# Performance work log

Measured on AMD Instinct MI355X. Metric: run time of the kernel, lower is better.

## Reference

```python
import jax, jax.numpy as jnp
import numpy as np

EMBD = 256
HEAD = 4
HD = EMBD // HEAD  # 64
EPS = 1e-5


def setup_inputs() -> dict:
    key = jax.random.key(0)
    ks = jax.random.split(key, 12)
    s = lambda fan_in: 1.0 / np.sqrt(fan_in)
    return {
        "x": jax.random.normal(ks[0], (16, 1024, EMBD), dtype=jnp.float32),
        # attention params (stored as [in, out])
        "qkv_w": jax.random.uniform(ks[1], (EMBD, 3 * EMBD), jnp.float32, -s(EMBD), s(EMBD)),
        "qkv_b": jax.random.uniform(ks[2], (3 * EMBD,), jnp.float32, -s(EMBD), s(EMBD)),
        "out_w": jax.random.uniform(ks[3], (EMBD, EMBD), jnp.float32, -s(EMBD), s(EMBD)),
        "out_b": jax.random.uniform(ks[4], (EMBD,), jnp.float32, -s(EMBD), s(EMBD)),
        # MLP params
        "fc_w": jax.random.uniform(ks[5], (EMBD, 4 * EMBD), jnp.float32, -s(EMBD), s(EMBD)),
        "fc_b": jax.random.uniform(ks[6], (4 * EMBD,), jnp.float32, -s(EMBD), s(EMBD)),
        "proj_w": jax.random.uniform(ks[7], (4 * EMBD, EMBD), jnp.float32, -s(4 * EMBD), s(4 * EMBD)),
        "proj_b": jax.random.uniform(ks[8], (EMBD,), jnp.float32, -s(4 * EMBD), s(4 * EMBD)),
        # LayerNorm params
        "ln1_g": jnp.ones((EMBD,), jnp.float32),
        "ln1_b": jnp.zeros((EMBD,), jnp.float32),
        "ln2_g": jnp.ones((EMBD,), jnp.float32),
        "ln2_b": jnp.zeros((EMBD,), jnp.float32),
    }


def layer_norm(x, g, b):
    mu = jnp.mean(x, axis=-1, keepdims=True)
    var = jnp.mean(jnp.square(x - mu), axis=-1, keepdims=True)
    return (x - mu) * jax.lax.rsqrt(var + EPS) * g + b


def block_forward(x, qkv_w, qkv_b, out_w, out_b, fc_w, fc_b, proj_w, proj_b,
                  ln1_g, ln1_b, ln2_g, ln2_b):
    B, S, E = x.shape
    # --- attention branch ---
    h = layer_norm(x, ln1_g, ln1_b)
    qkv = h @ qkv_w + qkv_b                       # [B,S,3E]
    q, k, v = jnp.split(qkv, 3, axis=-1)
    q = q.reshape(B, S, HEAD, HD).transpose(0, 2, 1, 3)  # [B,H,S,D]
    k = k.reshape(B, S, HEAD, HD).transpose(0, 2, 1, 3)
    v = v.reshape(B, S, HEAD, HD).transpose(0, 2, 1, 3)
    att = jnp.einsum('bhqd,bhkd->bhqk', q, k) / jnp.sqrt(jnp.float32(HD))
    causal = jnp.tril(jnp.ones((S, S), dtype=bool))
    att = jnp.where(causal, att, -jnp.inf)
    att = jax.nn.softmax(att, axis=-1)
    o = jnp.einsum('bhqk,bhkd->bhqd', att, v)     # [B,H,S,D]
    o = o.transpose(0, 2, 1, 3).reshape(B, S, E)
    x = x + o @ out_w + out_b
    # --- MLP branch (dropout inactive at eval) ---
    h = layer_norm(x, ln2_g, ln2_b)
    h = jax.nn.relu(h @ fc_w + fc_b)
    x = x + h @ proj_w + proj_b
    return x


def reference(x, qkv_w, qkv_b, out_w, out_b, fc_w, fc_b, proj_w, proj_b,
              ln1_g, ln1_b, ln2_g, ln2_b):
    return block_forward(x, qkv_w, qkv_b, out_w, out_b, fc_w, fc_b,
                         proj_w, proj_b, ln1_g, ln1_b, ln2_g, ln2_b)
```

## Files before the change

kernel.cpp:

```cpp
#include <hip/hip_runtime.h>
#include <cstdint>


using f32x4 = __attribute__((ext_vector_type(4))) float;
using s16x8 = __attribute__((ext_vector_type(8))) short;
using s16x4 = __attribute__((ext_vector_type(4))) short;

__device__ inline short f2bf(float f) {
    union { float f; unsigned u; } v{f};
    unsigned r = (v.u + 0x7FFFu + ((v.u >> 16) & 1u)) >> 16;
    return (short)r;
}

__device__ inline int cvt_pk_bf16(float lo, float hi) {
    int d;
    asm("v_cvt_pk_bf16_f32 %0, %1, %2" : "=v"(d) : "v"(lo), "v"(hi));
    return d;
}
__device__ inline void swap32(int& a, int& b) {
    asm("v_permlane32_swap_b32 %0, %1" : "+v"(a), "+v"(b));
}
__device__ inline void swap16(int& a, int& b) {
    asm("v_permlane16_swap_b32 %0, %1" : "+v"(a), "+v"(b));
}

__device__ inline void gload16(const void* g, void* l) {
    __builtin_amdgcn_global_load_lds(
        (const __attribute__((address_space(1))) void*)g,
        (__attribute__((address_space(3))) void*)l, 16, 0, 0);
}

__global__ __launch_bounds__(256) void wconv_all_kernel(
    const float* __restrict__ qkv_w, const float* __restrict__ out_w,
    const float* __restrict__ fc_w,  const float* __restrict__ proj_w,
    short* __restrict__ wt_qkv, short* __restrict__ wt_out,
    short* __restrict__ wt_fc,  short* __restrict__ wt_proj)
{
    __shared__ short T[64][65];
    int id = blockIdx.x;
    const float* W; short* Wt; int K, N, nt, kt;
    if (id < 48)       { W = qkv_w;  Wt = wt_qkv;  K = 256;  N = 768;  nt = id % 12;        kt = id / 12; }
    else if (id < 64)  { W = out_w;  Wt = wt_out;  K = 256;  N = 256;  nt = (id - 48) & 3;  kt = (id - 48) >> 2; }
    else if (id < 128) { W = fc_w;   Wt = wt_fc;   K = 256;  N = 1024; nt = (id - 64) & 15; kt = (id - 64) >> 4; }
    else               { W = proj_w; Wt = wt_proj; K = 1024; N = 256;  nt = (id - 128) & 3; kt = (id - 128) >> 2; }
    int n0 = nt * 64, k0 = kt * 64;

    int tid = threadIdx.x;
    int r  = tid >> 2;
    int c  = (tid & 3) << 4;

    const float* src = W + (size_t)(k0 + r) * N + n0 + c;
#pragma unroll
    for (int u = 0; u < 4; ++u) {
        float4 v = *reinterpret_cast<const float4*>(src + u * 4);
        T[r][c + u * 4 + 0] = f2bf(v.x);
        T[r][c + u * 4 + 1] = f2bf(v.y);
        T[r][c + u * 4 + 2] = f2bf(v.z);
        T[r][c + u * 4 + 3] = f2bf(v.w);
    }
    __syncthreads();
    s16x8 o0, o1;
#pragma unroll
    for (int j = 0; j < 8; ++j) { o0[j] = T[c + j][r]; o1[j] = T[c + 8 + j][r]; }
    short* dst = Wt + (size_t)(n0 + r) * K + k0 + c;
    *reinterpret_cast<s16x8*>(dst)     = o0;
    *reinterpret_cast<s16x8*>(dst + 8) = o1;
}

__global__ __launch_bounds__(256) void ln_kernel(const float* __restrict__ x,
                                                 const float* __restrict__ gamma,
                                                 const float* __restrict__ beta,
                                                 short* __restrict__ out)
{
    int tid  = threadIdx.x;
    int lane = tid & 63;
    int row  = blockIdx.x * 4 + (tid >> 6);
    const float* xr = x + (size_t)row * 256;
    float4 v = *reinterpret_cast<const float4*>(xr + lane * 4);

    float s = v.x + v.y + v.z + v.w;
#pragma unroll
    for (int o = 32; o >= 1; o >>= 1) s += __shfl_xor(s, o);
    float mu = s * (1.0f / 256.0f);

    float dx = v.x - mu, dy = v.y - mu, dz = v.z - mu, dw = v.w - mu;
    float q = dx * dx + dy * dy + dz * dz + dw * dw;
#pragma unroll
    for (int o = 32; o >= 1; o >>= 1) q += __shfl_xor(q, o);
    float rstd = rsqrtf(q * (1.0f / 256.0f) + 1e-5f);

    float4 gv = *reinterpret_cast<const float4*>(gamma + lane * 4);
    float4 bv = *reinterpret_cast<const float4*>(beta + lane * 4);
    s16x4 ov;
    ov[0] = f2bf(dx * rstd * gv.x + bv.x);
    ov[1] = f2bf(dy * rstd * gv.y + bv.y);
    ov[2] = f2bf(dz * rstd * gv.z + bv.z);
    ov[3] = f2bf(dw * rstd * gv.w + bv.w);
    *reinterpret_cast<s16x4*>(out + (size_t)row * 256 + lane * 4) = ov;
}

template <int RELU, int RES, int OBF16, int BM>
__global__ __launch_bounds__(256) void mgemm_kernel(const short* __restrict__ A,
                                                    const short* __restrict__ Bt,
                                                    const float* __restrict__ bias,
                                                    const float* __restrict__ R,
                                                    void* __restrict__ Cv,
                                                    int N, int K)
{
    constexpr int MI = BM / 32;
    __shared__ short As[BM * 64];
    __shared__ short Bs[128 * 64];

    int tid = threadIdx.x;
    int l   = tid & 63;
    int w   = tid >> 6;
    int lr  = l & 15;
    int lk8 = (l >> 4) << 3;
    int r4  = (l >> 4) << 2;
    int wr  = w >> 1, wc = w & 1;
    int bn  = blockIdx.x * 128, bm = blockIdx.y * BM;

    int scolS = ((l & 7) << 3) ^ ((l >> 3) << 3);
    int srowA = w * (BM / 4) + (l >> 3);
    int srowB = (w << 5) + (l >> 3);
    const short* pa = A  + (size_t)(bm + srowA) * K + scolS;
    const short* pb = Bt + (size_t)(bn + srowB) * K + scolS;
    short* dstA = As + w * (BM / 4) * 64;
    short* dstB = Bs + (w << 11);

    f32x4 acc[MI][4];
#pragma unroll
    for (int mi = 0; mi < MI; ++mi)
#pragma unroll
        for (int ni = 0; ni < 4; ++ni) acc[mi][ni] = (f32x4){0.f, 0.f, 0.f, 0.f};

    int swz = (lr & 7) << 3;

    for (int k0 = 0; k0 < K; k0 += 64) {
        __syncthreads();
#pragma unroll
        for (int i = 0; i < BM / 32; ++i)
            gload16(pa + (size_t)(i * 8) * K + k0, dstA + (i << 9));
#pragma unroll
        for (int i = 0; i < 4; ++i)
            gload16(pb + (size_t)(i * 8) * K + k0, dstB + (i << 9));
        __syncthreads();

#pragma unroll
        for (int ks = 0; ks < 2; ++ks) {
            s16x8 af[MI], bf[4];
#pragma unroll
            for (int mi = 0; mi < MI; ++mi) {
                int row = wr * (BM / 2) + (mi << 4) + lr;
                af[mi] = *reinterpret_cast<const s16x8*>(
                    &As[(row << 6) + (((ks << 5) + lk8) ^ swz)]);
            }
#pragma unroll
            for (int ni = 0; ni < 4; ++ni) {
                int row = (wc << 6) + (ni << 4) + lr;
                bf[ni] = *reinterpret_cast<const s16x8*>(
                    &Bs[(row << 6) + (((ks << 5) + lk8) ^ swz)]);
            }
#pragma unroll
            for (int mi = 0; mi < MI; ++mi)
#pragma unroll
                for (int ni = 0; ni < 4; ++ni)
                    acc[mi][ni] = __builtin_amdgcn_mfma_f32_16x16x32_bf16(
                        af[mi], bf[ni], acc[mi][ni], 0, 0, 0);
        }
    }

    float bv[4];
#pragma unroll
    for (int ni = 0; ni < 4; ++ni)
        bv[ni] = bias[bn + (wc << 6) + (ni << 4) + lr];

#pragma unroll
    for (int mi = 0; mi < MI; ++mi) {
#pragma unroll
        for (int ni = 0; ni < 4; ++ni) {
            int n = bn + (wc << 6) + (ni << 4) + lr;
#pragma unroll
            for (int r = 0; r < 4; ++r) {
                int m = bm + wr * (BM / 2) + (mi << 4) + r4 + r;
                float v = acc[mi][ni][r] + bv[ni];
                if (RELU) v = fmaxf(v, 0.0f);
                if (RES)  v += R[(size_t)m * N + n];
                if (OBF16) ((short*)Cv)[(size_t)m * N + n] = f2bf(v);
                else       ((float*)Cv)[(size_t)m * N + n] = v;
            }
        }
    }
}

__global__ __launch_bounds__(256) void oproj_ln_kernel(const short* __restrict__ A,
                                                       const short* __restrict__ Bt,
                                                       const float* __restrict__ bias,
                                                       const float* __restrict__ R,
                                                       float* __restrict__ x1,
                                                       short* __restrict__ h2,
                                                       const float* __restrict__ g,
                                                       const float* __restrict__ bb)
{
    __shared__ short As[64 * 64];
    __shared__ short Bs[256 * 64];

    int tid = threadIdx.x;
    int l   = tid & 63;
    int w   = tid >> 6;
    int lr  = l & 15;
    int lk8 = (l >> 4) << 3;
    int r4  = (l >> 4) << 2;
    int bm  = blockIdx.x * 64;

    int scolS = ((l & 7) << 3) ^ ((l >> 3) << 3);
    const short* pa = A  + (size_t)(bm + (w << 4) + (l >> 3)) * 256 + scolS;
    const short* pb = Bt + (size_t)((w << 6) + (l >> 3)) * 256 + scolS;
    short* dstA = As + (w << 10);
    short* dstB = Bs + (w << 12);

    f32x4 acc[16];
#pragma unroll
    for (int ni = 0; ni < 16; ++ni) acc[ni] = (f32x4){0.f, 0.f, 0.f, 0.f};

    int swz = (lr & 7) << 3;

    for (int k0 = 0; k0 < 256; k0 += 64) {
        __syncthreads();
#pragma unroll
        for (int i = 0; i < 2; ++i)
            gload16(pa + (size_t)(i * 8) * 256 + k0, dstA + (i << 9));
#pragma unroll
        for (int i = 0; i < 8; ++i)
            gload16(pb + (size_t)(i * 8) * 256 + k0, dstB + (i << 9));
        __syncthreads();

#pragma unroll
        for (int ks = 0; ks < 2; ++ks) {
            int arow = (w << 4) + lr;
            s16x8 af = *reinterpret_cast<const s16x8*>(
                &As[(arow << 6) + (((ks << 5) + lk8) ^ swz)]);
#pragma unroll
            for (int ni = 0; ni < 16; ++ni) {
                int row = (ni << 4) + lr;
                s16x8 bf = *reinterpret_cast<const s16x8*>(
                    &Bs[(row << 6) + (((ks << 5) + lk8) ^ swz)]);
                acc[ni] = __builtin_amdgcn_mfma_f32_16x16x32_bf16(af, bf, acc[ni], 0, 0, 0);
            }
        }
    }

#pragma unroll
    for (int ni = 0; ni < 16; ++ni) {
        int n = (ni << 4) + lr;
        float bvx = bias[n];
#pragma unroll
        for (int r = 0; r < 4; ++r) {
            int m = bm + (w << 4) + r4 + r;
            acc[ni][r] += bvx + R[(size_t)m * 256 + n];
        }
    }
#pragma unroll
    for (int r = 0; r < 4; ++r) {
        float s = 0.0f;
#pragma unroll
        for (int ni = 0; ni < 16; ++ni) s += acc[ni][r];
        s += __shfl_xor(s, 1); s += __shfl_xor(s, 2);
        s += __shfl_xor(s, 4); s += __shfl_xor(s, 8);
        float mu = s * (1.0f / 256.0f);
        float q = 0.0f;
#pragma unroll
        for (int ni = 0; ni < 16; ++ni) {
            float d = acc[ni][r] - mu;
            q += d * d;
        }
        q += __shfl_xor(q, 1); q += __shfl_xor(q, 2);
        q += __shfl_xor(q, 4); q += __shfl_xor(q, 8);
        float rstd = rsqrtf(q * (1.0f / 256.0f) + 1e-5f);

        int m = bm + (w << 4) + r4 + r;
#pragma unroll
        for (int ni = 0; ni < 16; ++ni) {
            int n = (ni << 4) + lr;
            float v = acc[ni][r];
            x1[(size_t)m * 256 + n] = v;
            h2[(size_t)m * 256 + n] = f2bf((v - mu) * rstd * g[n] + bb[n]);
        }
    }
}

__global__ __launch_bounds__(256, 4) void attn_kernel(const short* __restrict__ qkv,
                                                      short* __restrict__ o)
{
    __shared__ short Qs[64 * 64];
    __shared__ short Ks[128 * 64];
    __shared__ short Vt[2 * 64 * 64];

    int bid  = blockIdx.x;
    int xcd  = bid & 7;
    int rest = bid >> 3;
    int qt   = rest & 15;
    int bh   = ((rest >> 4) << 3) | xcd;
    int b = bh >> 2, h = bh & 3;

    int tid = threadIdx.x;
    const short* base = qkv + (size_t)b * 1024 * 768;

    int l   = tid & 63;
    int w   = tid >> 6;
    int lr  = l & 15;
    int g   = l >> 4;
    int lk8 = g << 3;
    int w16 = w << 4;
    int qglob = qt * 64 + w16 + lr;

    const float SC = 0.125f * 1.44269504088896f;

    {
        int qr = tid >> 2;
        int c0 = (tid & 3) << 4;
        int sw = (qr & 7) << 3;
        const short* qg = base + (size_t)(qt * 64 + qr) * 768 + h * 64 + c0;
        s16x8 q0 = *reinterpret_cast<const s16x8*>(qg);
        s16x8 q1 = *reinterpret_cast<const s16x8*>(qg + 8);
        *reinterpret_cast<s16x8*>(&Qs[qr * 64 + (c0 ^ sw)])       = q0;
        *reinterpret_cast<s16x8*>(&Qs[qr * 64 + ((c0 + 8) ^ sw)]) = q1;
    }
    __syncthreads();

    s16x8 qf[2];
#pragma unroll
    for (int ks = 0; ks < 2; ++ks) {
        int row = w16 + lr;
        qf[ks] = *reinterpret_cast<const s16x8*>(
            &Qs[row * 64 + ((32 * ks + lk8) ^ ((lr & 7) << 3))]);
    }

    float m = -1e30f, lsum = 0.0f;
    f32x4 oacc[4];
#pragma unroll
    for (int dt = 0; dt < 4; ++dt) oacc[dt] = (f32x4){0.f, 0.f, 0.f, 0.f};

    int ntile = qt >> 1;
    for (int kt = 0; kt <= ntile; ++kt) {
        __syncthreads();
        {
            int c0 = (tid & 3) << 4;
#pragma unroll
            for (int i = 0; i < 2; ++i) {
                int krow = i * 64 + (tid >> 2);
                const short* kg = base + (size_t)(kt * 128 + krow) * 768 + 256 + h * 64 + c0;
                s16x8 k0v = *reinterpret_cast<const s16x8*>(kg);
                s16x8 k1v = *reinterpret_cast<const s16x8*>(kg + 8);
                int sw = (krow & 7) << 3;
                *reinterpret_cast<s16x8*>(&Ks[krow * 64 + (c0 ^ sw)])       = k0v;
                *reinterpret_cast<s16x8*>(&Ks[krow * 64 + ((c0 + 8) ^ sw)]) = k1v;
                s16x8 v0 = *reinterpret_cast<const s16x8*>(kg + 256);
                s16x8 v1 = *reinterpret_cast<const s16x8*>(kg + 264);
                short* vth = Vt + ((krow >> 6) << 12);
                int kkl = krow & 63;
#pragma unroll
                for (int e = 0; e < 8; ++e) {
                    int da = c0 + e, db = c0 + 8 + e;
                    vth[da * 64 + (kkl ^ ((da & 7) << 3))] = v0[e];
                    vth[db * 64 + (kkl ^ ((db & 7) << 3))] = v1[e];
                }
            }
        }
        __syncthreads();

        f32x4 s[8];
#pragma unroll
        for (int jt = 0; jt < 8; ++jt) s[jt] = (f32x4){0.f, 0.f, 0.f, 0.f};
#pragma unroll
        for (int ks = 0; ks < 2; ++ks) {
#pragma unroll
            for (int jt = 0; jt < 8; ++jt) {
                int row = jt * 16 + lr;
                s16x8 kf = *reinterpret_cast<const s16x8*>(
                    &Ks[row * 64 + ((32 * ks + lk8) ^ ((lr & 7) << 3))]);
                s[jt] = __builtin_amdgcn_mfma_f32_16x16x32_bf16(kf, qf[ks], s[jt], 0, 0, 0);
            }
        }
#pragma unroll
        for (int jt = 0; jt < 8; ++jt)
#pragma unroll
            for (int r = 0; r < 4; ++r) s[jt][r] *= SC;

        if (kt == ntile) {
#pragma unroll
            for (int jt = 0; jt < 8; ++jt) {
                int kb = kt * 128 + jt * 16 + 4 * g;
#pragma unroll
                for (int r = 0; r < 4; ++r)
                    if (kb + r > qglob) s[jt][r] = -1e30f;
            }
        }

        float rm = fmaxf(fmaxf(s[0][0], s[0][1]), fmaxf(s[0][2], s[0][3]));
#pragma unroll
        for (int jt = 1; jt < 8; ++jt) {
            float t = fmaxf(fmaxf(s[jt][0], s[jt][1]), fmaxf(s[jt][2], s[jt][3]));
            rm = fmaxf(rm, t);
        }
        rm = fmaxf(rm, __shfl_xor(rm, 16));
        rm = fmaxf(rm, __shfl_xor(rm, 32));
        float mn  = fmaxf(m, rm);
        float fct = exp2f(m - mn);
        m = mn;
        float ps = 0.0f;
#pragma unroll
        for (int jt = 0; jt < 8; ++jt) {
#pragma unroll
            for (int r = 0; r < 4; ++r) {
                float p = exp2f(s[jt][r] - mn);
                s[jt][r] = p;
                ps += p;
            }
        }
        ps += __shfl_xor(ps, 16);
        ps += __shfl_xor(ps, 32);
        lsum = lsum * fct + ps;

        int cpk[8][2];
#pragma unroll
        for (int jt = 0; jt < 8; ++jt) {
            cpk[jt][0] = cvt_pk_bf16(s[jt][0], s[jt][1]);
            cpk[jt][1] = cvt_pk_bf16(s[jt][2], s[jt][3]);
        }

#pragma unroll
        for (int r = 0; r < 4; ++r) {
            float f4 = __shfl(fct, 4 * g + r);
#pragma unroll
            for (int dt = 0; dt < 4; ++dt) oacc[dt][r] *= f4;
        }

#pragma unroll
        for (int ks = 0; ks < 4; ++ks) {
            int a0 = cpk[2 * ks][0],     a1 = cpk[2 * ks][1];
            int b0 = cpk[2 * ks + 1][0], b1 = cpk[2 * ks + 1][1];
            swap32(a0, b0); swap32(a1, b1);
            swap16(a0, b0); swap16(a1, b1);
            union { int i[4]; s16x8 v; } fr;
            fr.i[0] = a0; fr.i[1] = a1; fr.i[2] = b0; fr.i[3] = b1;
            const short* vth = Vt + ((ks >> 1) << 12);
#pragma unroll
            for (int dt = 0; dt < 4; ++dt) {
                int vrow = dt * 16 + lr;
                s16x8 vf = *reinterpret_cast<const s16x8*>(
                    &vth[vrow * 64 + ((((ks & 1) << 5) + lk8) ^ ((lr & 7) << 3))]);
                oacc[dt] = __builtin_amdgcn_mfma_f32_16x16x32_bf16(fr.v, vf, oacc[dt], 0, 0, 0);
            }
        }
    }

#pragma unroll
    for (int r = 0; r < 4; ++r) {
        float lv  = __shfl(lsum, 4 * g + r);
        float inv = 1.0f / lv;
        short* orow = o + (size_t)(b * 1024 + qt * 64 + w16 + 4 * g + r) * 256 + h * 64;
#pragma unroll
        for (int dt = 0; dt < 4; ++dt)
            orow[dt * 16 + lr] = f2bf(oacc[dt][r] * inv);
    }
}

extern "C" void kernel_launch(void* const* d_in, const int* in_sizes, int n_in,
                              void* d_out, int out_size, void* d_ws, size_t ws_size,
                              hipStream_t stream)
{
    const float* x      = (const float*)d_in[0];
    const float* qkv_w  = (const float*)d_in[1];
    const float* qkv_b  = (const float*)d_in[2];
    const float* out_w  = (const float*)d_in[3];
    const float* out_b  = (const float*)d_in[4];
    const float* fc_w   = (const float*)d_in[5];
    const float* fc_b   = (const float*)d_in[6];
    const float* proj_w = (const float*)d_in[7];
    const float* proj_b = (const float*)d_in[8];
    const float* ln1_g  = (const float*)d_in[9];
    const float* ln1_b  = (const float*)d_in[10];
    const float* ln2_g  = (const float*)d_in[11];
    const float* ln2_b  = (const float*)d_in[12];
    float* out = (float*)d_out;

    short* ws = (short*)d_ws;
    short* wt_qkv  = ws;
    short* wt_out  = ws + 196608;
    short* wt_fc   = ws + 262144;
    short* wt_proj = ws + 524288;
    short* bufA    = ws + 786432;
    short* bufB    = ws + 4980736;

    dim3 blk(256);

    wconv_all_kernel<<<dim3(192), blk, 0, stream>>>(
        qkv_w, out_w, fc_w, proj_w, wt_qkv, wt_out, wt_fc, wt_proj);
    ln_kernel<<<dim3(4096), blk, 0, stream>>>(x, ln1_g, ln1_b, bufA);
    mgemm_kernel<0, 0, 1, 128><<<dim3(6, 128), blk, 0, stream>>>(
        bufA, wt_qkv, qkv_b, nullptr, bufB, 768, 256);
    attn_kernel<<<dim3(1024), blk, 0, stream>>>(bufB, bufA);
    oproj_ln_kernel<<<dim3(256), blk, 0, stream>>>(
        bufA, wt_out, out_b, x, out, bufA, ln2_g, ln2_b);
    mgemm_kernel<1, 0, 1, 128><<<dim3(8, 128), blk, 0, stream>>>(
        bufA, wt_fc, fc_b, nullptr, bufB, 1024, 256);
    mgemm_kernel<0, 1, 0, 64><<<dim3(2, 256), blk, 0, stream>>>(
        bufB, wt_proj, proj_b, out, out, 256, 1024);
}
```

Baseline: 137.6 us.

## Restructure causal attention with pre-transposed V, paired q-tiles, and double-buffered K/V

The QKV GEMM epilogue now writes Q/K into a 512-wide buffer and V directly transposed per head. This removes the scalar in-kernel V transpose into LDS. The attention kernel processes a balanced pair of query tiles (qt and 15-qt) per block and reads Q fragments straight from global memory. It uses 64-key tiles double-buffered in LDS via async global-to-LDS loads (gload16) so the next tile's load overlaps compute. The costs are fewer blocks, lower occupancy (launch bounds 2), and strided scattered bf16 stores for V in the GEMM epilogue.

```diff
diff --git a/kernel.cpp b/kernel.cpp
--- a/kernel.cpp
+++ b/kernel.cpp
@@ -99,12 +99,13 @@
     *reinterpret_cast<s16x4*>(out + (size_t)row * 256 + lane * 4) = ov;
 }
 
-template <int RELU, int RES, int OBF16, int BM>
+template <int RELU, int RES, int OBF16, int BM, int QKV>
 __global__ __launch_bounds__(256) void mgemm_kernel(const short* __restrict__ A,
                                                     const short* __restrict__ Bt,
                                                     const float* __restrict__ bias,
                                                     const float* __restrict__ R,
                                                     void* __restrict__ Cv,
+                                                    short* __restrict__ vt,
                                                     int N, int K)
 {
     constexpr int MI = BM / 32;
@@ -186,8 +187,19 @@
                 float v = acc[mi][ni][r] + bv[ni];
                 if (RELU) v = fmaxf(v, 0.0f);
                 if (RES)  v += R[(size_t)m * N + n];
-                if (OBF16) ((short*)Cv)[(size_t)m * N + n] = f2bf(v);
-                else       ((float*)Cv)[(size_t)m * N + n] = v;
+                if (QKV) {
+                    if (bn < 512) {
+                        ((short*)Cv)[(size_t)m * 512 + n] = f2bf(v);
+                    } else {
+                        int hh = (n - 512) >> 6, dd = (n - 512) & 63;
+                        int bb = m >> 10, ss = m & 1023;
+                        vt[(size_t)((((bb << 2) | hh) << 6) | dd) * 1024 + ss] = f2bf(v);
+                    }
+                } else if (OBF16) {
+                    ((short*)Cv)[(size_t)m * N + n] = f2bf(v);
+                } else {
+                    ((float*)Cv)[(size_t)m * N + n] = v;
+                }
             }
         }
     }
@@ -289,180 +301,169 @@
     }
 }
 
-__global__ __launch_bounds__(256, 4) void attn_kernel(const short* __restrict__ qkv,
+__global__ __launch_bounds__(256, 2) void attn_kernel(const short* __restrict__ qk,
+                                                      const short* __restrict__ vt,
                                                       short* __restrict__ o)
 {
-    __shared__ short Qs[64 * 64];
-    __shared__ short Ks[128 * 64];
-    __shared__ short Vt[2 * 64 * 64];
+    __shared__ short Ks[2][64 * 64];
+    __shared__ short Vs[2][64 * 64];
 
     int bid  = blockIdx.x;
     int xcd  = bid & 7;
-    int rest = bid >> 3;
-    int qt   = rest & 15;
-    int bh   = ((rest >> 4) << 3) | xcd;
+    int pair = (bid >> 3) & 7;
+    int bhg  = bid >> 6;
+    int bh   = (bhg << 3) | xcd;
     int b = bh >> 2, h = bh & 3;
 
     int tid = threadIdx.x;
-    const short* base = qkv + (size_t)b * 1024 * 768;
-
     int l   = tid & 63;
     int w   = tid >> 6;
     int lr  = l & 15;
     int g   = l >> 4;
     int lk8 = g << 3;
     int w16 = w << 4;
-    int qglob = qt * 64 + w16 + lr;
+
+    int srow = (w << 3) + (l >> 3);
+    int scol = ((l & 7) << 3) ^ (((l >> 3) & 7) << 3);
+    const short* kgp = qk + (size_t)(b * 1024 + srow) * 512 + 256 + h * 64 + scol;
+    const short* vgp = vt + (size_t)((bh << 6) + srow) * 1024 + scol;
+    short* dstK = &Ks[0][(w << 3) * 64];
+    short* dstV = &Vs[0][(w << 3) * 64];
+    const int BUFS = 64 * 64;
 
     const float SC = 0.125f * 1.44269504088896f;
-
-    {
-        int qr = tid >> 2;
-        int c0 = (tid & 3) << 4;
-        int sw = (qr & 7) << 3;
-        const short* qg = base + (size_t)(qt * 64 + qr) * 768 + h * 64 + c0;
-        s16x8 q0 = *reinterpret_cast<const s16x8*>(qg);
-        s16x8 q1 = *reinterpret_cast<const s16x8*>(qg + 8);
-        *reinterpret_cast<s16x8*>(&Qs[qr * 64 + (c0 ^ sw)])       = q0;
-        *reinterpret_cast<s16x8*>(&Qs[qr * 64 + ((c0 + 8) ^ sw)]) = q1;
-    }
-    __syncthreads();
-
-    s16x8 qf[2];
-#pragma unroll
-    for (int ks = 0; ks < 2; ++ks) {
-        int row = w16 + lr;
-        qf[ks] = *reinterpret_cast<const s16x8*>(
-            &Qs[row * 64 + ((32 * ks + lk8) ^ ((lr & 7) << 3))]);
-    }
-
-    float m = -1e30f, lsum = 0.0f;
-    f32x4 oacc[4];
-#pragma unroll
-    for (int dt = 0; dt < 4; ++dt) oacc[dt] = (f32x4){0.f, 0.f, 0.f, 0.f};
-
-    int ntile = qt >> 1;
-    for (int kt = 0; kt <= ntile; ++kt) {
+    int rsw = (lr & 7) << 3;
+
+    int cur = 1;
+    for (int sel = 0; sel < 2; ++sel) {
+        int qt = sel == 0 ? pair : 15 - pair;
+
+        const short* qrow = qk + (size_t)(b * 1024 + qt * 64 + w16 + lr) * 512 + h * 64;
+        s16x8 qf[2];
+        qf[0] = *reinterpret_cast<const s16x8*>(qrow + lk8);
+        qf[1] = *reinterpret_cast<const s16x8*>(qrow + 32 + lk8);
+
+#pragma unroll
+        for (int i = 0; i < 2; ++i) {
+            gload16(kgp + (size_t)(qt * 0 + i * 32) * 512, dstK + (cur ^ 1) * BUFS + (i << 11));
+            gload16(vgp + (size_t)(i * 32) * 1024,         dstV + (cur ^ 1) * BUFS + (i << 11));
+        }
         __syncthreads();
-        {
-            int c0 = (tid & 3) << 4;
-#pragma unroll
-            for (int i = 0; i < 2; ++i) {
-                int krow = i * 64 + (tid >> 2);
-                const short* kg = base + (size_t)(kt * 128 + krow) * 768 + 256 + h * 64 + c0;
-                s16x8 k0v = *reinterpret_cast<const s16x8*>(kg);
-                s16x8 k1v = *reinterpret_cast<const s16x8*>(kg + 8);
-                int sw = (krow & 7) << 3;
-                *reinterpret_cast<s16x8*>(&Ks[krow * 64 + (c0 ^ sw)])       = k0v;
-                *reinterpret_cast<s16x8*>(&Ks[krow * 64 + ((c0 + 8) ^ sw)]) = k1v;
-                s16x8 v0 = *reinterpret_cast<const s16x8*>(kg + 256);
-                s16x8 v1 = *reinterpret_cast<const s16x8*>(kg + 264);
-                short* vth = Vt + ((krow >> 6) << 12);
-                int kkl = krow & 63;
-#pragma unroll
-                for (int e = 0; e < 8; ++e) {
-                    int da = c0 + e, db = c0 + 8 + e;
-                    vth[da * 64 + (kkl ^ ((da & 7) << 3))] = v0[e];
-                    vth[db * 64 + (kkl ^ ((db & 7) << 3))] = v1[e];
+        cur ^= 1;
+
+        float m = -1e30f, lsum = 0.0f;
+        f32x4 oacc[4];
+#pragma unroll
+        for (int dt = 0; dt < 4; ++dt) oacc[dt] = (f32x4){0.f, 0.f, 0.f, 0.f};
+        int qglob = qt * 64 + w16 + lr;
+
+        for (int kt = 0; kt <= qt; ++kt) {
+            if (kt < qt) {
+#pragma unroll
+                for (int i = 0; i < 2; ++i) {
+                    gload16(kgp + (size_t)((kt + 1) * 64 + i * 32) * 512,
+                            dstK + (cur ^ 1) * BUFS + (i << 11));
+                    gload16(vgp + (size_t)(i * 32) * 1024 + (kt + 1) * 64,
+                            dstV + (cur ^ 1) * BUFS + (i << 11));
                 }
             }
-        }
-        __syncthreads();
-
-        f32x4 s[8];
-#pragma unroll
-        for (int jt = 0; jt < 8; ++jt) s[jt] = (f32x4){0.f, 0.f, 0.f, 0.f};
-#pragma unroll
-        for (int ks = 0; ks < 2; ++ks) {
-#pragma unroll
-            for (int jt = 0; jt < 8; ++jt) {
-                int row = jt * 16 + lr;
-                s16x8 kf = *reinterpret_cast<const s16x8*>(
-                    &Ks[row * 64 + ((32 * ks + lk8) ^ ((lr & 7) << 3))]);
-                s[jt] = __builtin_amdgcn_mfma_f32_16x16x32_bf16(kf, qf[ks], s[jt], 0, 0, 0);
-            }
-        }
-#pragma unroll
-        for (int jt = 0; jt < 8; ++jt)
-#pragma unroll
-            for (int r = 0; r < 4; ++r) s[jt][r] *= SC;
-
-        if (kt == ntile) {
-#pragma unroll
-            for (int jt = 0; jt < 8; ++jt) {
-                int kb = kt * 128 + jt * 16 + 4 * g;
-#pragma unroll
-                for (int r = 0; r < 4; ++r)
-                    if (kb + r > qglob) s[jt][r] = -1e30f;
-            }
-        }
-
-        float rm = fmaxf(fmaxf(s[0][0], s[0][1]), fmaxf(s[0][2], s[0][3]));
-#pragma unroll
-        for (int jt = 1; jt < 8; ++jt) {
-            float t = fmaxf(fmaxf(s[jt][0], s[jt][1]), fmaxf(s[jt][2], s[jt][3]));
-            rm = fmaxf(rm, t);
-        }
-        rm = fmaxf(rm, __shfl_xor(rm, 16));
-        rm = fmaxf(rm, __shfl_xor(rm, 32));
-        float mn  = fmaxf(m, rm);
-        float fct = exp2f(m - mn);
-        m = mn;
-        float ps = 0.0f;
-#pragma unroll
-        for (int jt = 0; jt < 8; ++jt) {
+
+            f32x4 s[4];
+#pragma unroll
+            for (int jt = 0; jt < 4; ++jt) s[jt] = (f32x4){0.f, 0.f, 0.f, 0.f};
+#pragma unroll
+            for (int ks = 0; ks < 2; ++ks) {
+#pragma unroll
+                for (int jt = 0; jt < 4; ++jt) {
+                    int row = jt * 16 + lr;
+                    s16x8 kf = *reinterpret_cast<const s16x8*>(
+                        &Ks[cur][(row << 6) + ((32 * ks + lk8) ^ rsw)]);
+                    s[jt] = __builtin_amdgcn_mfma_f32_16x16x32_bf16(kf, qf[ks], s[jt], 0, 0, 0);
+                }
+            }
+#pragma unroll
+            for (int jt = 0; jt < 4; ++jt)
+#pragma unroll
+                for (int r = 0; r < 4; ++r) s[jt][r] *= SC;
+
+            if (kt == qt) {
+#pragma unroll
+                for (int jt = 0; jt < 4; ++jt) {
+                    int kb = kt * 64 + jt * 16 + (g << 2);
+#pragma unroll
+                    for (int r = 0; r < 4; ++r)
+                        if (kb + r > qglob) s[jt][r] = -1e30f;
+                }
+            }
+
+            float rm = fmaxf(fmaxf(s[0][0], s[0][1]), fmaxf(s[0][2], s[0][3]));
+#pragma unroll
+            for (int jt = 1; jt < 4; ++jt)
+                rm = fmaxf(rm, fmaxf(fmaxf(s[jt][0], s[jt][1]), fmaxf(s[jt][2], s[jt][3])));
+            rm = fmaxf(rm, __shfl_xor(rm, 16));
+            rm = fmaxf(rm, __shfl_xor(rm, 32));
+            float mn  = fmaxf(m, rm);
+            float fct = exp2f(m - mn);
+            m = mn;
+            float ps = 0.0f;
+#pragma unroll
+            for (int jt = 0; jt < 4; ++jt)
+#pragma unroll
+                for (int r = 0; r < 4; ++r) {
+                    float p = exp2f(s[jt][r] - mn);
+                    s[jt][r] = p;
+                    ps += p;
+                }
+            ps += __shfl_xor(ps, 16);
+            ps += __shfl_xor(ps, 32);
+            lsum = lsum * fct + ps;
+
+            int cpk[4][2];
+#pragma unroll
+            for (int jt = 0; jt < 4; ++jt) {
+                cpk[jt][0] = cvt_pk_bf16(s[jt][0], s[jt][1]);
+                cpk[jt][1] = cvt_pk_bf16(s[jt][2], s[jt][3]);
+            }
+
 #pragma unroll
             for (int r = 0; r < 4; ++r) {
-                float p = exp2f(s[jt][r] - mn);
-                s[jt][r] = p;
-                ps += p;
-            }
-        }
-        ps += __shfl_xor(ps, 16);
-        ps += __shfl_xor(ps, 32);
-        lsum = lsum * fct + ps;
-
-        int cpk[8][2];
-#pragma unroll
-        for (int jt = 0; jt < 8; ++jt) {
-            cpk[jt][0] = cvt_pk_bf16(s[jt][0], s[jt][1]);
-            cpk[jt][1] = cvt_pk_bf16(s[jt][2], s[jt][3]);
+                float f4 = __shfl(fct, 4 * g + r);
+#pragma unroll
+                for (int dt = 0; dt < 4; ++dt) oacc[dt][r] *= f4;
+            }
+
+#pragma unroll
+            for (int ks = 0; ks < 2; ++ks) {
+                int a0 = cpk[2 * ks][0],     a1 = cpk[2 * ks][1];
+                int b0 = cpk[2 * ks + 1][0], b1 = cpk[2 * ks + 1][1];
+                swap32(a0, b0); swap32(a1, b1);
+                swap16(a0, b0); swap16(a1, b1);
+                union { int i[4]; s16x8 v; } fr;
+                fr.i[0] = a0; fr.i[1] = a1; fr.i[2] = b0; fr.i[3] = b1;
+#pragma unroll
+                for (int dt = 0; dt < 4; ++dt) {
+                    int row = dt * 16 + lr;
+                    s16x8 vf = *reinterpret_cast<const s16x8*>(
+                        &Vs[cur][(row << 6) + ((32 * ks + lk8) ^ rsw)]);
+                    oacc[dt] = __builtin_amdgcn_mfma_f32_16x16x32_bf16(fr.v, vf, oacc[dt], 0, 0, 0);
+                }
+            }
+
+            if (kt < qt) {
+                __syncthreads();
+                cur ^= 1;
+            }
         }
 
 #pragma unroll
         for (int r = 0; r < 4; ++r) {
-            float f4 = __shfl(fct, 4 * g + r);
-#pragma unroll
-            for (int dt = 0; dt < 4; ++dt) oacc[dt][r] *= f4;
-        }
-
-#pragma unroll
-        for (int ks = 0; ks < 4; ++ks) {
-            int a0 = cpk[2 * ks][0],     a1 = cpk[2 * ks][1];
-            int b0 = cpk[2 * ks + 1][0], b1 = cpk[2 * ks + 1][1];
-            swap32(a0, b0); swap32(a1, b1);
-            swap16(a0, b0); swap16(a1, b1);
-            union { int i[4]; s16x8 v; } fr;
-            fr.i[0] = a0; fr.i[1] = a1; fr.i[2] = b0; fr.i[3] = b1;
-            const short* vth = Vt + ((ks >> 1) << 12);
-#pragma unroll
-            for (int dt = 0; dt < 4; ++dt) {
-                int vrow = dt * 16 + lr;
-                s16x8 vf = *reinterpret_cast<const s16x8*>(
-                    &vth[vrow * 64 + ((((ks & 1) << 5) + lk8) ^ ((lr & 7) << 3))]);
-                oacc[dt] = __builtin_amdgcn_mfma_f32_16x16x32_bf16(fr.v, vf, oacc[dt], 0, 0, 0);
-            }
-        }
-    }
-
-#pragma unroll
-    for (int r = 0; r < 4; ++r) {
-        float lv  = __shfl(lsum, 4 * g + r);
-        float inv = 1.0f / lv;
-        short* orow = o + (size_t)(b * 1024 + qt * 64 + w16 + 4 * g + r) * 256 + h * 64;
-#pragma unroll
-        for (int dt = 0; dt < 4; ++dt)
-            orow[dt * 16 + lr] = f2bf(oacc[dt][r] * inv);
+            float lv  = __shfl(lsum, 4 * g + r);
+            float inv = 1.0f / lv;
+            short* orow = o + (size_t)(b * 1024 + qt * 64 + w16 + 4 * g + r) * 256 + h * 64;
+#pragma unroll
+            for (int dt = 0; dt < 4; ++dt)
+                orow[dt * 16 + lr] = f2bf(oacc[dt][r] * inv);
+        }
     }
 }
 
@@ -491,20 +492,22 @@
     short* wt_fc   = ws + 262144;
     short* wt_proj = ws + 524288;
     short* bufA    = ws + 786432;
-    short* bufB    = ws + 4980736;
+    short* qk_buf  = ws + 4980736;
+    short* vt_buf  = ws + 13369344;
+    short* h3_buf  = ws + 4980736;
 
     dim3 blk(256);
 
     wconv_all_kernel<<<dim3(192), blk, 0, stream>>>(
         qkv_w, out_w, fc_w, proj_w, wt_qkv, wt_out, wt_fc, wt_proj);
     ln_kernel<<<dim3(4096), blk, 0, stream>>>(x, ln1_g, ln1_b, bufA);
-    mgemm_kernel<0, 0, 1, 128><<<dim3(6, 128), blk, 0, stream>>>(
-        bufA, wt_qkv, qkv_b, nullptr, bufB, 768, 256);
-    attn_kernel<<<dim3(1024), blk, 0, stream>>>(bufB, bufA);
+    mgemm_kernel<0, 0, 1, 128, 1><<<dim3(6, 128), blk, 0, stream>>>(
+        bufA, wt_qkv, qkv_b, nullptr, qk_buf, vt_buf, 768, 256);
+    attn_kernel<<<dim3(512), blk, 0, stream>>>(qk_buf, vt_buf, bufA);
     oproj_ln_kernel<<<dim3(256), blk, 0, stream>>>(
         bufA, wt_out, out_b, x, out, bufA, ln2_g, ln2_b);
-    mgemm_kernel<1, 0, 1, 128><<<dim3(8, 128), blk, 0, stream>>>(
-        bufA, wt_fc, fc_b, nullptr, bufB, 1024, 256);
-    mgemm_kernel<0, 1, 0, 64><<<dim3(2, 256), blk, 0, stream>>>(
-        bufB, wt_proj, proj_b, out, out, 256, 1024);
-}
+    mgemm_kernel<1, 0, 1, 128, 0><<<dim3(8, 128), blk, 0, stream>>>(
+        bufA, wt_fc, fc_b, nullptr, h3_buf, nullptr, 1024, 256);
+    mgemm_kernel<0, 1, 0, 64, 0><<<dim3(2, 256), blk, 0, stream>>>(
+        h3_buf, wt_proj, proj_b, out, out, nullptr, 256, 1024);
+}
```

Result: faster. 125.4 us (-8.9%).
